# Kernel tuning notes

Hardware: AMD Instinct MI355X
Metric: run time of the kernel (lower is better)

## Reference

```python
import jax, jax.numpy as jnp
import numpy as np

D_MODEL = 1024
N_HEADS = 16
HEAD_DIM = D_MODEL // N_HEADS
ROPE_BASE = 10000.0


def rotate_half(x):
    x1, x2 = x[..., : x.shape[-1] // 2], x[..., x.shape[-1] // 2 :]
    return jnp.concatenate((-x2, x1), axis=-1)


def rope_cos_sin(L, dim, dtype):
    inv_freq = 1.0 / (ROPE_BASE ** (jnp.arange(0, dim, 2, dtype=jnp.float32) / dim))
    freqs = jnp.arange(L, dtype=jnp.float32)[:, None] * inv_freq[None, :]  # [L, dim/2]
    emb = jnp.concatenate((freqs, freqs), axis=-1)  # [L, dim]
    # broadcast over batch and heads: [1, L, 1, dim]
    return jnp.cos(emb)[None, :, None, :].astype(dtype), jnp.sin(emb)[None, :, None, :].astype(dtype)


def setup_inputs() -> dict:
    key = jax.random.key(0)
    ks = jax.random.split(key, 11)
    N, L, S = 2, 2048, 2048
    s = 1.0 / np.sqrt(D_MODEL)
    return {
        "queries": jax.random.normal(ks[0], (N, L, D_MODEL), jnp.float32),
        "keys": jax.random.normal(ks[1], (N, S, D_MODEL), jnp.float32),
        "values": jax.random.normal(ks[2], (N, S, D_MODEL), jnp.float32),
        "Wq": jax.random.normal(ks[3], (D_MODEL, D_MODEL), jnp.float32) * s,
        "bq": jnp.zeros((D_MODEL,), jnp.float32),
        "Wk": jax.random.normal(ks[4], (D_MODEL, D_MODEL), jnp.float32) * s,
        "bk": jnp.zeros((D_MODEL,), jnp.float32),
        "Wv": jax.random.normal(ks[5], (D_MODEL, D_MODEL), jnp.float32) * s,
        "bv": jnp.zeros((D_MODEL,), jnp.float32),
        "Wo": jax.random.normal(ks[6], (D_MODEL, D_MODEL), jnp.float32) * s,
        "bo": jnp.zeros((D_MODEL,), jnp.float32),
    }


def reference(queries, keys, values, Wq, bq, Wk, bk, Wv, bv, Wo, bo):
    N, L, _ = queries.shape
    S = keys.shape[1]
    H, hd = N_HEADS, HEAD_DIM

    # QKV projections (nn.Linear: x @ W.T + b), reshape to [N, T, H, hd]
    q = (jnp.einsum("nld,ed->nle", queries, Wq) + bq).reshape(N, L, H, hd)
    k = (jnp.einsum("nsd,ed->nse", keys, Wk) + bk).reshape(N, S, H, hd)
    v = (jnp.einsum("nsd,ed->nse", values, Wv) + bv).reshape(N, S, H, hd)

    # Rotary embedding: q*cos + rotate_half(q)*sin  (same for k)
    cos, sin = rope_cos_sin(L, hd, q.dtype)
    q = q * cos + rotate_half(q) * sin
    k = k * cos + rotate_half(k) * sin

    # Inner attention: scaled dot-product with causal mask
    scores = jnp.einsum("nlhd,nshd->nhls", q, k) / jnp.sqrt(jnp.asarray(hd, q.dtype))
    causal = jnp.tril(jnp.ones((L, S), bool))
    scores = jnp.where(causal[None, None], scores, jnp.asarray(-1e9, scores.dtype))
    attn = jax.nn.softmax(scores, axis=-1)
    out = jnp.einsum("nhls,nshd->nlhd", attn, v).reshape(N, L, H * hd)

    # Output projection
    return jnp.einsum("nle,de->nld", out, Wo) + bo
```

## Files before the change

### kernel.cpp

```cpp
#include <hip/hip_runtime.h>
#include <math.h>

#define DM 1024
#define NH 16
#define HD 64
#define SEQ 2048
#define NB2 2
#define MROWS 4096

typedef unsigned short u16;
typedef __attribute__((ext_vector_type(8))) short short8;
typedef __attribute__((ext_vector_type(4))) float f32x4;
typedef __attribute__((ext_vector_type(2))) unsigned int u32x2;

#define GLOAD16(g, l) __builtin_amdgcn_global_load_lds( \
    (const __attribute__((address_space(1))) void*)(g),  \
    (__attribute__((address_space(3))) void*)(l), 16, 0, 0)

static __device__ __forceinline__ u16 f2bf(float f) {
  union { float f; unsigned u; } v; v.f = f;
  unsigned r = v.u + 0x7fffu + ((v.u >> 16) & 1u);
  return (u16)(r >> 16);
}

static __device__ __forceinline__ short8 cvt8(float4 a, float4 b) {
  short8 s;
  s[0] = (short)f2bf(a.x); s[1] = (short)f2bf(a.y);
  s[2] = (short)f2bf(a.z); s[3] = (short)f2bf(a.w);
  s[4] = (short)f2bf(b.x); s[5] = (short)f2bf(b.y);
  s[6] = (short)f2bf(b.z); s[7] = (short)f2bf(b.w);
  return s;
}

__global__ void conv_all(
    const float* __restrict__ q, const float* __restrict__ k, const float* __restrict__ v,
    const float* __restrict__ wq, const float* __restrict__ wk,
    const float* __restrict__ wv, const float* __restrict__ wo,
    u16* __restrict__ xq, u16* __restrict__ xk, u16* __restrict__ xv,
    u16* __restrict__ wqb, u16* __restrict__ wkb, u16* __restrict__ wvb, u16* __restrict__ wob,
    float* __restrict__ cosT, float* __restrict__ sinT)
{
  const int z = blockIdx.z;
  const int idx = blockIdx.x * blockDim.x + threadIdx.x;
  if (z == 7) {
    if (idx >= SEQ * 32) return;
    int l = idx >> 5, i = idx & 31;
    float invf = expf(-(float)i * (9.210340371976184f / 32.0f));
    float ang = (float)l * invf;
    float s, c;
    sincosf(ang, &s, &c);
    cosT[idx] = c; sinT[idx] = s;
    return;
  }
  const float* src; u16* dst; int n;
  switch (z) {
    case 0: src = q;  dst = xq;  n = MROWS * DM; break;
    case 1: src = k;  dst = xk;  n = MROWS * DM; break;
    case 2: src = v;  dst = xv;  n = MROWS * DM; break;
    case 3: src = wq; dst = wqb; n = DM * DM; break;
    case 4: src = wk; dst = wkb; n = DM * DM; break;
    case 5: src = wv; dst = wvb; n = DM * DM; break;
    default: src = wo; dst = wob; n = DM * DM; break;
  }
  const int base = idx * 8;
  if (base >= n) return;
  float4 a = *(const float4*)(src + base);
  float4 b = *(const float4*)(src + base + 4);
  *(short8*)(dst + base) = cvt8(a, b);
}

__global__ __launch_bounds__(512) void gemm_qkv(
    const u16* __restrict__ Xq, const u16* __restrict__ Xk, const u16* __restrict__ Xv,
    const u16* __restrict__ Wqb, const u16* __restrict__ Wkb, const u16* __restrict__ Wvb,
    const float* __restrict__ bq, const float* __restrict__ bk, const float* __restrict__ bv,
    u16* __restrict__ Qb, u16* __restrict__ Kb, u16* __restrict__ VT,
    const float* __restrict__ cosT, const float* __restrict__ sinT)
{
  __shared__ __align__(16) u16 SH[49152];
  const int z = blockIdx.z;
  const u16* A = (z == 0) ? Xq : (z == 1) ? Xk : Xv;
  const u16* W = (z == 0) ? Wqb : (z == 1) ? Wkb : Wvb;
  const float* bias = (z == 0) ? bq : (z == 1) ? bk : bv;
  const int row0 = blockIdx.x * 256, col0 = blockIdx.y * 256;

  const int tid = threadIdx.x;
  const int lane = tid & 63;
  const int wid = tid >> 6;
  const int wm = wid >> 2;
  const int wn = wid & 3;
  const int fr = lane & 15, kg = lane >> 4;

  const u16* ga = A + (size_t)(row0 + (tid & 255)) * DM + ((tid >> 8) << 3);
  const u16* gb = W + (size_t)(col0 + (tid & 255)) * DM + ((tid >> 8) << 3);
  const int lw = (wid >> 2) * 2048 + (wid & 3) * 512;
  u16* B0 = SH;
  u16* B1 = SH + 16384;
  u16* B2 = SH + 32768;

  f32x4 acc[8][4];
#pragma unroll
  for (int m = 0; m < 8; ++m)
#pragma unroll
    for (int n = 0; n < 4; ++n) acc[m][n] = (f32x4){0.f, 0.f, 0.f, 0.f};

  auto issue = [&](int t, u16* buf) {
    const int ko = t * 32;
    GLOAD16(ga + ko, buf + lw);
    GLOAD16(ga + ko + 16, buf + lw + 4096);
    GLOAD16(gb + ko, buf + 8192 + lw);
    GLOAD16(gb + ko + 16, buf + 8192 + lw + 4096);
  };
  auto compute = [&](const u16* buf) {
    short8 afr[8], bfr[4];
#pragma unroll
    for (int m = 0; m < 8; ++m)
      afr[m] = *(const short8*)(&buf[kg * 2048 + (wm * 128 + m * 16 + fr) * 8]);
#pragma unroll
    for (int n = 0; n < 4; ++n)
      bfr[n] = *(const short8*)(&buf[8192 + kg * 2048 + (wn * 64 + n * 16 + fr) * 8]);
    __builtin_amdgcn_s_setprio(1);
#pragma unroll
    for (int m = 0; m < 8; ++m)
#pragma unroll
      for (int n = 0; n < 4; ++n)
        acc[m][n] = __builtin_amdgcn_mfma_f32_16x16x32_bf16(afr[m], bfr[n], acc[m][n], 0, 0, 0);
    __builtin_amdgcn_s_setprio(0);
  };

  issue(0, B0);
  issue(1, B1);

#define STEP4(t, bufR, bufW) do {                                   \
    asm volatile("s_waitcnt vmcnt(4)" ::: "memory");                \
    __builtin_amdgcn_sched_barrier(0);                              \
    __builtin_amdgcn_s_barrier();                                   \
    __builtin_amdgcn_sched_barrier(0);                              \
    if ((t) + 2 < 32) issue((t) + 2, bufW);                         \
    compute(bufR);                                                  \
  } while (0)
#define STEP0(t, bufR) do {                                         \
    asm volatile("s_waitcnt vmcnt(0)" ::: "memory");                \
    __builtin_amdgcn_sched_barrier(0);                              \
    __builtin_amdgcn_s_barrier();                                   \
    __builtin_amdgcn_sched_barrier(0);                              \
    compute(bufR);                                                  \
  } while (0)

  for (int t = 0; t < 30; t += 3) {
    STEP4(t,     B0, B2);
    STEP4(t + 1, B1, B0);
    STEP4(t + 2, B2, B1);
  }
  STEP4(30, B0, B2);
  STEP0(31, B1);
#undef STEP4
#undef STEP0

  if (z == 2) {
    __syncthreads();
    const int nb = row0 >> 11;
    const int sbase = row0 & (SEQ - 1);
#pragma unroll
    for (int p = 0; p < 4; ++p) {
      if (wn == p) {
#pragma unroll
        for (int n = 0; n < 4; ++n) {
          const int dcol = n * 16 + fr;
          const float bv = bias[col0 + p * 64 + dcol];
#pragma unroll
          for (int m = 0; m < 8; ++m)
#pragma unroll
            for (int r = 0; r < 4; ++r)
              SH[dcol * 264 + wm * 128 + m * 16 + kg * 4 + r] = f2bf(acc[m][n][r] + bv);
        }
      }
      __syncthreads();
      {
        const int dcol = tid >> 3, sq = tid & 7;
        const int e = col0 + p * 64 + dcol;
        u16* dst = VT + ((size_t)(nb * NH + (e >> 6)) * HD + (e & 63)) * SEQ + sbase + sq * 32;
#pragma unroll
        for (int j = 0; j < 4; ++j)
          *(short8*)(dst + j * 8) = *(const short8*)(&SH[dcol * 264 + sq * 32 + j * 8]);
      }
      __syncthreads();
    }
    return;
  }

  const float qscale = (z == 0) ? 0.125f : 1.0f;
  u16* Cb = (z == 0) ? Qb : Kb;
#pragma unroll
  for (int m = 0; m < 8; ++m) {
#pragma unroll
    for (int r = 0; r < 4; ++r) {
      const int rowg = row0 + wm * 128 + m * 16 + kg * 4 + r;
      const int l = rowg & (SEQ - 1);
#pragma unroll
      for (int n = 0; n < 4; ++n) {
        const int colg = col0 + wn * 64 + n * 16 + fr;
        const int i = n * 16 + fr;
        const int fi = i & 31;
        const float c = cosT[l * 32 + fi];
        const float s = sinT[l * 32 + fi];
        const float v = acc[m][n][r] + bias[colg];
        const float pv = acc[m][n ^ 2][r] + bias[col0 + wn * 64 + ((n ^ 2) * 16 + fr)];
        const float o = v * c + ((i < 32) ? -pv : pv) * s;
        Cb[(size_t)rowg * DM + colg] = f2bf(o * qscale);
      }
    }
  }
}

__global__ __launch_bounds__(512) void gemm_o(
    const u16* __restrict__ Ob, const u16* __restrict__ Wob,
    const float* __restrict__ bo, float* __restrict__ out)
{
  __shared__ __align__(16) u16 SH[32768];
  const int row0 = blockIdx.x * 128, col0 = blockIdx.y * 128;
  const int tid = threadIdx.x;
  const int lane = tid & 63;
  const int wid = tid >> 6;
  const int wr = wid & 3;
  const int wc = wid >> 2;
  const int fr = lane & 15, kg = lane >> 4;

  const u16* ga = Ob + (size_t)(row0 + (tid & 127)) * DM + ((tid >> 7) << 3);
  const u16* gb = Wob + (size_t)(col0 + (tid & 127)) * DM + ((tid >> 7) << 3);
  const int lw = wid * 512;
  u16* B0 = SH;
  u16* B1 = SH + 16384;

  f32x4 acc[2][4];
#pragma unroll
  for (int m = 0; m < 2; ++m)
#pragma unroll
    for (int n = 0; n < 4; ++n) acc[m][n] = (f32x4){0.f, 0.f, 0.f, 0.f};

  auto issue = [&](int t, u16* buf) {
    const int ko = t * 64;
    GLOAD16(ga + ko, buf + lw);
    GLOAD16(ga + ko + 32, buf + lw + 4096);
    GLOAD16(gb + ko, buf + 8192 + lw);
    GLOAD16(gb + ko + 32, buf + 8192 + lw + 4096);
  };
  auto compute = [&](const u16* buf, int kk) {
    const int kc = kk * 4 + kg;
    short8 afr[2], bfr[4];
#pragma unroll
    for (int m = 0; m < 2; ++m)
      afr[m] = *(const short8*)(&buf[kc * 1024 + (wr * 32 + m * 16 + fr) * 8]);
#pragma unroll
    for (int n = 0; n < 4; ++n)
      bfr[n] = *(const short8*)(&buf[8192 + kc * 1024 + (wc * 64 + n * 16 + fr) * 8]);
    __builtin_amdgcn_s_setprio(1);
#pragma unroll
    for (int m = 0; m < 2; ++m)
#pragma unroll
      for (int n = 0; n < 4; ++n)
        acc[m][n] = __builtin_amdgcn_mfma_f32_16x16x32_bf16(afr[m], bfr[n], acc[m][n], 0, 0, 0);
    __builtin_amdgcn_s_setprio(0);
  };

  issue(0, B0);
  const int KT = DM / 64;
  for (int t = 0; t < KT; ++t) {
    u16* bufR = (t & 1) ? B1 : B0;
    u16* bufW = (t & 1) ? B0 : B1;
    __syncthreads();
    if (t + 1 < KT) issue(t + 1, bufW);
    compute(bufR, 0);
    compute(bufR, 1);
  }

#pragma unroll
  for (int m = 0; m < 2; ++m) {
#pragma unroll
    for (int r = 0; r < 4; ++r) {
      const int rowg = row0 + wr * 32 + m * 16 + kg * 4 + r;
#pragma unroll
      for (int n = 0; n < 4; ++n) {
        const int colg = col0 + wc * 64 + n * 16 + fr;
        out[(size_t)rowg * DM + colg] = acc[m][n][r] + bo[colg];
      }
    }
  }
}

__global__ __launch_bounds__(512) void flash_attn(
    const u16* __restrict__ Qp, const u16* __restrict__ Kp,
    const u16* __restrict__ VT, u16* __restrict__ Op)
{
  __shared__ __align__(16) u16 Ks[4096];
  __shared__ __align__(16) u16 Vt[4096];
  __shared__ __align__(16) u16 Pl[9216];

  const int tid = threadIdx.x;
  const int lane = tid & 63;
  const int w = tid >> 6;
  const int fr = lane & 15, rg = lane >> 4;
  const int qbp = blockIdx.x;
  const int h = blockIdx.y, nb = blockIdx.z;

  const size_t headoff = (size_t)nb * SEQ * DM + (size_t)h * HD;
  const size_t vthead = (size_t)(nb * NH + h) * HD * SEQ;
  const int srow = tid >> 3;
  const int sch  = tid & 7;
  u16* Pw = &Pl[w * 1152];

  for (int pass = 0; pass < 2; ++pass) {
    const int qe = pass ? (15 - qbp) : qbp;
    const int KBend = 2 * qe + 2;
    const int qrow0 = qe * 128 + w * 16;
    const int qg = qrow0 + fr;

    short8 qf[2];
#pragma unroll
    for (int ck = 0; ck < 2; ++ck)
      qf[ck] = *(const short8*)(Qp + headoff + (size_t)(qrow0 + fr) * DM + ck * 32 + rg * 8);

    f32x4 accO[4];
#pragma unroll
    for (int df = 0; df < 4; ++df) accO[df] = (f32x4){0.f, 0.f, 0.f, 0.f};
    float m_run = -3e38f, l_run = 0.f;

    short8 kpf = *(const short8*)(Kp + headoff + (size_t)srow * DM + sch * 8);
    short8 vpf = *(const short8*)(VT + vthead + (size_t)srow * SEQ + sch * 8);

    for (int kb = 0; kb < KBend; ++kb) {
      *(short8*)(&Ks[(sch * 64 + (srow ^ sch)) * 8]) = kpf;
      *(short8*)(&Vt[(sch * 64 + (srow ^ sch)) * 8]) = vpf;
      __syncthreads();
      if (kb + 1 < KBend) {
        kpf = *(const short8*)(Kp + headoff + (size_t)((kb + 1) * 64 + srow) * DM + sch * 8);
        vpf = *(const short8*)(VT + vthead + (size_t)srow * SEQ + (kb + 1) * 64 + sch * 8);
      }

      const bool active = (kb * 64) <= (qrow0 + 15);
      if (active) {
        short8 kf[4][2];
#pragma unroll
        for (int sf = 0; sf < 4; ++sf)
#pragma unroll
          for (int ck = 0; ck < 2; ++ck) {
            const int dc = ck * 4 + rg;
            kf[sf][ck] = *(const short8*)(&Ks[(dc * 64 + ((sf * 16 + fr) ^ dc)) * 8]);
          }
        f32x4 sc_[4];
#pragma unroll
        for (int sf = 0; sf < 4; ++sf) {
          f32x4 z = (f32x4){0.f, 0.f, 0.f, 0.f};
#pragma unroll
          for (int ck = 0; ck < 2; ++ck)
            z = __builtin_amdgcn_mfma_f32_16x16x32_bf16(kf[sf][ck], qf[ck], z, 0, 0, 0);
          sc_[sf] = z;
        }
        float rowmax = -3e38f;
#pragma unroll
        for (int sf = 0; sf < 4; ++sf)
#pragma unroll
          for (int r = 0; r < 4; ++r) {
            const int sg = kb * 64 + sf * 16 + rg * 4 + r;
            float v = sc_[sf][r];
            v = (sg <= qg) ? v : -3e38f;
            sc_[sf][r] = v;
            rowmax = fmaxf(rowmax, v);
          }
        rowmax = fmaxf(rowmax, __shfl_xor(rowmax, 16, 64));
        rowmax = fmaxf(rowmax, __shfl_xor(rowmax, 32, 64));
        const float mnew = fmaxf(m_run, rowmax);
        const float scl = __expf(m_run - mnew);
        m_run = mnew;
        float psum = 0.f;
#pragma unroll
        for (int sf = 0; sf < 4; ++sf)
#pragma unroll
          for (int r = 0; r < 4; ++r) {
            const float p = __expf(sc_[sf][r] - mnew);
            sc_[sf][r] = p;
            psum += p;
          }
        psum += __shfl_xor(psum, 16, 64);
        psum += __shfl_xor(psum, 32, 64);
        l_run = l_run * scl + psum;
        const float s0 = __shfl(scl, rg * 4 + 0, 64);
        const float s1 = __shfl(scl, rg * 4 + 1, 64);
        const float s2 = __shfl(scl, rg * 4 + 2, 64);
        const float s3 = __shfl(scl, rg * 4 + 3, 64);
#pragma unroll
        for (int df = 0; df < 4; ++df) {
          accO[df][0] *= s0; accO[df][1] *= s1;
          accO[df][2] *= s2; accO[df][3] *= s3;
        }
#pragma unroll
        for (int sf = 0; sf < 4; ++sf) {
          u32x2 pv;
          pv[0] = (unsigned)f2bf(sc_[sf][0]) | ((unsigned)f2bf(sc_[sf][1]) << 16);
          pv[1] = (unsigned)f2bf(sc_[sf][2]) | ((unsigned)f2bf(sc_[sf][3]) << 16);
          *(u32x2*)(&Pw[fr * 72 + (sf * 8 + rg * 2) * 2]) = pv;
        }
        short8 pa[2];
#pragma unroll
        for (int ck = 0; ck < 2; ++ck)
          pa[ck] = *(const short8*)(&Pw[fr * 72 + (ck * 16 + rg * 4) * 2]);
#pragma unroll
        for (int df = 0; df < 4; ++df)
#pragma unroll
          for (int ck = 0; ck < 2; ++ck) {
            const int sc = ck * 4 + rg;
            const short8 vf = *(const short8*)(&Vt[(sc * 64 + ((df * 16 + fr) ^ sc)) * 8]);
            accO[df] = __builtin_amdgcn_mfma_f32_16x16x32_bf16(pa[ck], vf, accO[df], 0, 0, 0);
          }
      }
      __syncthreads();
    }

    const float l0 = __shfl(l_run, rg * 4 + 0, 64);
    const float l1 = __shfl(l_run, rg * 4 + 1, 64);
    const float l2 = __shfl(l_run, rg * 4 + 2, 64);
    const float l3 = __shfl(l_run, rg * 4 + 3, 64);
#pragma unroll
    for (int df = 0; df < 4; ++df) {
      const int d = df * 16 + fr;
      Op[headoff + (size_t)(qrow0 + rg * 4 + 0) * DM + d] = f2bf(accO[df][0] / l0);
      Op[headoff + (size_t)(qrow0 + rg * 4 + 1) * DM + d] = f2bf(accO[df][1] / l1);
      Op[headoff + (size_t)(qrow0 + rg * 4 + 2) * DM + d] = f2bf(accO[df][2] / l2);
      Op[headoff + (size_t)(qrow0 + rg * 4 + 3) * DM + d] = f2bf(accO[df][3] / l3);
    }
  }
}

extern "C" void kernel_launch(void* const* d_in, const int* in_sizes, int n_in,
                              void* d_out, int out_size, void* d_ws, size_t ws_size,
                              hipStream_t stream) {
  (void)in_sizes; (void)n_in; (void)out_size; (void)ws_size;
  const float* queries = (const float*)d_in[0];
  const float* keys    = (const float*)d_in[1];
  const float* values  = (const float*)d_in[2];
  const float* Wq = (const float*)d_in[3];
  const float* bq = (const float*)d_in[4];
  const float* Wk = (const float*)d_in[5];
  const float* bk = (const float*)d_in[6];
  const float* Wv = (const float*)d_in[7];
  const float* bv = (const float*)d_in[8];
  const float* Wo = (const float*)d_in[9];
  const float* bo = (const float*)d_in[10];
  float* out = (float*)d_out;

  char* ws = (char*)d_ws;
  const size_t MB = 1u << 20;
  u16* Qb  = (u16*)(ws);
  u16* Kb  = (u16*)(ws + 8 * MB);
  u16* VTg = (u16*)(ws + 16 * MB);
  u16* Xq  = (u16*)(ws + 24 * MB);
  u16* Ob  = Xq;
  u16* Xk  = (u16*)(ws + 32 * MB);
  u16* Xv  = (u16*)(ws + 40 * MB);
  u16* Wqb = (u16*)(ws + 48 * MB);
  u16* Wkb = (u16*)(ws + 50 * MB);
  u16* Wvb = (u16*)(ws + 52 * MB);
  u16* Wob = (u16*)(ws + 54 * MB);
  float* cosT = (float*)(ws + 56 * MB);
  float* sinT = (float*)(ws + 56 * MB + 256 * 1024);

  conv_all<<<dim3(2048, 1, 8), 256, 0, stream>>>(
      queries, keys, values, Wq, Wk, Wv, Wo,
      Xq, Xk, Xv, Wqb, Wkb, Wvb, Wob, cosT, sinT);
  gemm_qkv<<<dim3(MROWS / 256, DM / 256, 3), 512, 0, stream>>>(
      Xq, Xk, Xv, Wqb, Wkb, Wvb, bq, bk, bv, Qb, Kb, VTg, cosT, sinT);
  flash_attn<<<dim3(SEQ / 256, NH, NB2), 512, 0, stream>>>(Qb, Kb, VTg, Ob);
  gemm_o<<<dim3(MROWS / 128, DM / 128), 512, 0, stream>>>(Ob, Wob, bo, out);
}
```

Before: 148.4 us.

## Split GEMM mainloops into ping-pong half-phases with staggered A/B loads

Result: faster. 142.1 us (-4.3%).

```diff
diff --git a/kernel.cpp b/kernel.cpp
--- a/kernel.cpp
+++ b/kernel.cpp
@@ -103,58 +103,79 @@
 #pragma unroll
     for (int n = 0; n < 4; ++n) acc[m][n] = (f32x4){0.f, 0.f, 0.f, 0.f};
 
-  auto issue = [&](int t, u16* buf) {
+  auto issueA = [&](int t, u16* buf) {
     const int ko = t * 32;
     GLOAD16(ga + ko, buf + lw);
     GLOAD16(ga + ko + 16, buf + lw + 4096);
+  };
+  auto issueB = [&](int t, u16* buf) {
+    const int ko = t * 32;
     GLOAD16(gb + ko, buf + 8192 + lw);
     GLOAD16(gb + ko + 16, buf + 8192 + lw + 4096);
   };
-  auto compute = [&](const u16* buf) {
-    short8 afr[8], bfr[4];
-#pragma unroll
-    for (int m = 0; m < 8; ++m)
-      afr[m] = *(const short8*)(&buf[kg * 2048 + (wm * 128 + m * 16 + fr) * 8]);
+
+  auto phA = [&](const u16* bufR, u16* bufW, int t2, short8* bfr) {
+    short8 afr[4];
+#pragma unroll
+    for (int m = 0; m < 4; ++m)
+      afr[m] = *(const short8*)(&bufR[kg * 2048 + (wm * 128 + m * 16 + fr) * 8]);
 #pragma unroll
     for (int n = 0; n < 4; ++n)
-      bfr[n] = *(const short8*)(&buf[8192 + kg * 2048 + (wn * 64 + n * 16 + fr) * 8]);
+      bfr[n] = *(const short8*)(&bufR[8192 + kg * 2048 + (wn * 64 + n * 16 + fr) * 8]);
+    if (t2 < 32) issueA(t2, bufW);
+    __builtin_amdgcn_sched_barrier(0);
+    __builtin_amdgcn_s_barrier();
+    __builtin_amdgcn_sched_barrier(0);
     __builtin_amdgcn_s_setprio(1);
 #pragma unroll
-    for (int m = 0; m < 8; ++m)
+    for (int m = 0; m < 4; ++m)
 #pragma unroll
       for (int n = 0; n < 4; ++n)
         acc[m][n] = __builtin_amdgcn_mfma_f32_16x16x32_bf16(afr[m], bfr[n], acc[m][n], 0, 0, 0);
     __builtin_amdgcn_s_setprio(0);
-  };
-
-  issue(0, B0);
-  issue(1, B1);
-
-#define STEP4(t, bufR, bufW) do {                                   \
-    asm volatile("s_waitcnt vmcnt(4)" ::: "memory");                \
+    __builtin_amdgcn_sched_barrier(0);
+    __builtin_amdgcn_s_barrier();
+    __builtin_amdgcn_sched_barrier(0);
+  };
+  auto phB = [&](const u16* bufR, u16* bufW, int t2, const short8* bfr) {
+    short8 afr[4];
+#pragma unroll
+    for (int m = 0; m < 4; ++m)
+      afr[m] = *(const short8*)(&bufR[kg * 2048 + (wm * 128 + (m + 4) * 16 + fr) * 8]);
+    if (t2 < 32) issueB(t2, bufW);
+    __builtin_amdgcn_sched_barrier(0);
+    __builtin_amdgcn_s_barrier();
+    __builtin_amdgcn_sched_barrier(0);
+    __builtin_amdgcn_s_setprio(1);
+#pragma unroll
+    for (int m = 0; m < 4; ++m)
+#pragma unroll
+      for (int n = 0; n < 4; ++n)
+        acc[m + 4][n] = __builtin_amdgcn_mfma_f32_16x16x32_bf16(afr[m], bfr[n], acc[m + 4][n], 0, 0, 0);
+    __builtin_amdgcn_s_setprio(0);
+  };
+
+  issueA(0, B0); issueB(0, B0);
+  issueA(1, B1); issueB(1, B1);
+
+#define QSTEP(WLIT, bufR, bufW, t2) do {                            \
+    asm volatile("s_waitcnt vmcnt(" WLIT ")" ::: "memory");         \
     __builtin_amdgcn_sched_barrier(0);                              \
     __builtin_amdgcn_s_barrier();                                   \
     __builtin_amdgcn_sched_barrier(0);                              \
-    if ((t) + 2 < 32) issue((t) + 2, bufW);                         \
-    compute(bufR);                                                  \
+    short8 bfr[4];                                                  \
+    phA(bufR, bufW, t2, bfr);                                       \
+    phB(bufR, bufW, t2, bfr);                                       \
   } while (0)
-#define STEP0(t, bufR) do {                                         \
-    asm volatile("s_waitcnt vmcnt(0)" ::: "memory");                \
-    __builtin_amdgcn_sched_barrier(0);                              \
-    __builtin_amdgcn_s_barrier();                                   \
-    __builtin_amdgcn_sched_barrier(0);                              \
-    compute(bufR);                                                  \
-  } while (0)
 
   for (int t = 0; t < 30; t += 3) {
-    STEP4(t,     B0, B2);
-    STEP4(t + 1, B1, B0);
-    STEP4(t + 2, B2, B1);
-  }
-  STEP4(30, B0, B2);
-  STEP0(31, B1);
-#undef STEP4
-#undef STEP0
+    QSTEP("4", B0, B2, t + 2);
+    QSTEP("4", B1, B0, t + 3);
+    QSTEP("4", B2, B1, t + 4);
+  }
+  QSTEP("4", B0, B2, 32);
+  QSTEP("0", B1, B2, 33);
+#undef QSTEP
 
   if (z == 2) {
     __syncthreads();
@@ -212,47 +233,55 @@
   }
 }
 
-__global__ __launch_bounds__(512) void gemm_o(
+__global__ __launch_bounds__(256) void gemm_o(
     const u16* __restrict__ Ob, const u16* __restrict__ Wob,
     const float* __restrict__ bo, float* __restrict__ out)
 {
-  __shared__ __align__(16) u16 SH[32768];
+  __shared__ __align__(16) u16 SH[24576];
   const int row0 = blockIdx.x * 128, col0 = blockIdx.y * 128;
   const int tid = threadIdx.x;
   const int lane = tid & 63;
-  const int wid = tid >> 6;
-  const int wr = wid & 3;
-  const int wc = wid >> 2;
+  const int w = tid >> 6;
+  const int wr = w >> 1;
+  const int wc = w & 1;
   const int fr = lane & 15, kg = lane >> 4;
 
   const u16* ga = Ob + (size_t)(row0 + (tid & 127)) * DM + ((tid >> 7) << 3);
   const u16* gb = Wob + (size_t)(col0 + (tid & 127)) * DM + ((tid >> 7) << 3);
-  const int lw = wid * 512;
+  const int lw = w * 512;
   u16* B0 = SH;
-  u16* B1 = SH + 16384;
-
-  f32x4 acc[2][4];
-#pragma unroll
-  for (int m = 0; m < 2; ++m)
+  u16* B1 = SH + 8192;
+  u16* B2 = SH + 16384;
+
+  f32x4 acc[4][4];
+#pragma unroll
+  for (int m = 0; m < 4; ++m)
 #pragma unroll
     for (int n = 0; n < 4; ++n) acc[m][n] = (f32x4){0.f, 0.f, 0.f, 0.f};
 
-  auto issue = [&](int t, u16* buf) {
-    const int ko = t * 64;
+  auto issueA = [&](int t, u16* buf) {
+    const int ko = t * 32;
     GLOAD16(ga + ko, buf + lw);
-    GLOAD16(ga + ko + 32, buf + lw + 4096);
-    GLOAD16(gb + ko, buf + 8192 + lw);
-    GLOAD16(gb + ko + 32, buf + 8192 + lw + 4096);
-  };
-  auto compute = [&](const u16* buf, int kk) {
-    const int kc = kk * 4 + kg;
-    short8 afr[2], bfr[4];
+    GLOAD16(ga + ko + 16, buf + lw + 2048);
+  };
+  auto issueB = [&](int t, u16* buf) {
+    const int ko = t * 32;
+    GLOAD16(gb + ko, buf + 4096 + lw);
+    GLOAD16(gb + ko + 16, buf + 4096 + lw + 2048);
+  };
+
+  auto phA = [&](const u16* bufR, u16* bufW, int t2, short8* bfr) {
+    short8 afr[2];
 #pragma unroll
     for (int m = 0; m < 2; ++m)
-      afr[m] = *(const short8*)(&buf[kc * 1024 + (wr * 32 + m * 16 + fr) * 8]);
+      afr[m] = *(const short8*)(&bufR[kg * 1024 + (wr * 64 + m * 16 + fr) * 8]);
 #pragma unroll
     for (int n = 0; n < 4; ++n)
-      bfr[n] = *(const short8*)(&buf[8192 + kc * 1024 + (wc * 64 + n * 16 + fr) * 8]);
+      bfr[n] = *(const short8*)(&bufR[4096 + kg * 1024 + (wc * 64 + n * 16 + fr) * 8]);
+    if (t2 < 32) issueA(t2, bufW);
+    __builtin_amdgcn_sched_barrier(0);
+    __builtin_amdgcn_s_barrier();
+    __builtin_amdgcn_sched_barrier(0);
     __builtin_amdgcn_s_setprio(1);
 #pragma unroll
     for (int m = 0; m < 2; ++m)
@@ -260,24 +289,55 @@
       for (int n = 0; n < 4; ++n)
         acc[m][n] = __builtin_amdgcn_mfma_f32_16x16x32_bf16(afr[m], bfr[n], acc[m][n], 0, 0, 0);
     __builtin_amdgcn_s_setprio(0);
-  };
-
-  issue(0, B0);
-  const int KT = DM / 64;
-  for (int t = 0; t < KT; ++t) {
-    u16* bufR = (t & 1) ? B1 : B0;
-    u16* bufW = (t & 1) ? B0 : B1;
-    __syncthreads();
-    if (t + 1 < KT) issue(t + 1, bufW);
-    compute(bufR, 0);
-    compute(bufR, 1);
-  }
-
-#pragma unroll
-  for (int m = 0; m < 2; ++m) {
+    __builtin_amdgcn_sched_barrier(0);
+    __builtin_amdgcn_s_barrier();
+    __builtin_amdgcn_sched_barrier(0);
+  };
+  auto phB = [&](const u16* bufR, u16* bufW, int t2, const short8* bfr) {
+    short8 afr[2];
+#pragma unroll
+    for (int m = 0; m < 2; ++m)
+      afr[m] = *(const short8*)(&bufR[kg * 1024 + (wr * 64 + (m + 2) * 16 + fr) * 8]);
+    if (t2 < 32) issueB(t2, bufW);
+    __builtin_amdgcn_sched_barrier(0);
+    __builtin_amdgcn_s_barrier();
+    __builtin_amdgcn_sched_barrier(0);
+    __builtin_amdgcn_s_setprio(1);
+#pragma unroll
+    for (int m = 0; m < 2; ++m)
+#pragma unroll
+      for (int n = 0; n < 4; ++n)
+        acc[m + 2][n] = __builtin_amdgcn_mfma_f32_16x16x32_bf16(afr[m], bfr[n], acc[m + 2][n], 0, 0, 0);
+    __builtin_amdgcn_s_setprio(0);
+  };
+
+  issueA(0, B0); issueB(0, B0);
+  issueA(1, B1); issueB(1, B1);
+
+#define OSTEP(WLIT, bufR, bufW, t2) do {                            \
+    asm volatile("s_waitcnt vmcnt(" WLIT ")" ::: "memory");         \
+    __builtin_amdgcn_sched_barrier(0);                              \
+    __builtin_amdgcn_s_barrier();                                   \
+    __builtin_amdgcn_sched_barrier(0);                              \
+    short8 bfr[4];                                                  \
+    phA(bufR, bufW, t2, bfr);                                       \
+    phB(bufR, bufW, t2, bfr);                                       \
+  } while (0)
+
+  for (int t = 0; t < 30; t += 3) {
+    OSTEP("4", B0, B2, t + 2);
+    OSTEP("4", B1, B0, t + 3);
+    OSTEP("4", B2, B1, t + 4);
+  }
+  OSTEP("4", B0, B2, 32);
+  OSTEP("0", B1, B2, 33);
+#undef OSTEP
+
+#pragma unroll
+  for (int m = 0; m < 4; ++m) {
 #pragma unroll
     for (int r = 0; r < 4; ++r) {
-      const int rowg = row0 + wr * 32 + m * 16 + kg * 4 + r;
+      const int rowg = row0 + wr * 64 + m * 16 + kg * 4 + r;
 #pragma unroll
       for (int n = 0; n < 4; ++n) {
         const int colg = col0 + wc * 64 + n * 16 + fr;
@@ -469,5 +529,5 @@
   gemm_qkv<<<dim3(MROWS / 256, DM / 256, 3), 512, 0, stream>>>(
       Xq, Xk, Xv, Wqb, Wkb, Wvb, bq, bk, bv, Qb, Kb, VTg, cosT, sinT);
   flash_attn<<<dim3(SEQ / 256, NH, NB2), 512, 0, stream>>>(Qb, Kb, VTg, Ob);
-  gemm_o<<<dim3(MROWS / 128, DM / 128), 512, 0, stream>>>(Ob, Wob, bo, out);
-}
+  gemm_o<<<dim3(MROWS / 128, DM / 128), 512 / 2, 0, stream>>>(Ob, Wob, bo, out);
+}
```
